# Kernel optimization log

Hardware: AMD Instinct MI355X
Metric: run time of the kernel (lower is better)

## Reference

```python
import jax, jax.numpy as jnp
import numpy as np

DILATIONS = [1, 2, 4, 8, 16, 32, 64, 128, 256, 512] * 2
WD = 128   # residual/gate channels
SD = 512   # skip channels
VOCAB = 256
FIELD = int(np.sum(DILATIONS)) + 2  # receptive field = 2048


def setup_inputs() -> dict:
    key = jax.random.key(0)
    ks = jax.random.split(key, 10)
    B, T = 4, 16384
    L = len(DILATIONS)
    y = jax.random.randint(ks[0], (B, T), 0, VOCAB)
    embed = jax.random.normal(ks[1], (VOCAB, WD), dtype=jnp.float32) * 0.1
    # dilated causal conv: kernel_size=2, wd -> 2*wd (gate stacking)
    Wd = jax.random.normal(ks[2], (L, 2 * WD, WD, 2), dtype=jnp.float32) * 0.05
    bd = jnp.zeros((L, 2 * WD), dtype=jnp.float32)
    # skip 1x1 conv: wd -> sd
    Ws = jax.random.normal(ks[3], (L, SD, WD, 1), dtype=jnp.float32) * 0.05
    bs = jnp.zeros((L, SD), dtype=jnp.float32)
    # residual 1x1 conv: wd -> wd
    Wr = jax.random.normal(ks[4], (L, WD, WD, 1), dtype=jnp.float32) * 0.05
    br = jnp.zeros((L, WD), dtype=jnp.float32)
    # post convs (bias=False)
    W1 = jax.random.normal(ks[5], (SD, SD, 1), dtype=jnp.float32) * 0.05
    W2 = jax.random.normal(ks[6], (VOCAB, SD, 1), dtype=jnp.float32) * 0.05
    return {"y": y, "embed": embed, "Wd": Wd, "bd": bd, "Ws": Ws,
            "bs": bs, "Wr": Wr, "br": br, "W1": W1, "W2": W2}


def reference(y, embed, Wd, bd, Ws, bs, Wr, br, W1, W2):
    # embedding -> [B, C, T]
    x = jnp.transpose(embed[y], (0, 2, 1))
    finalout = x.shape[2] - (FIELD - 1)
    skip = None
    for i, d in enumerate(DILATIONS):
        # dilated valid conv with kernel size 2 == two shifted 1x1 matmuls
        in_act = (jnp.einsum('oc,bct->bot', Wd[i, :, :, 0], x[:, :, :-d]) +
                  jnp.einsum('oc,bct->bot', Wd[i, :, :, 1], x[:, :, d:]) +
                  bd[i][None, :, None])                       # [B, 2*WD, T-d]
        acts = jnp.tanh(in_act[:, :WD]) * jax.nn.sigmoid(in_act[:, WD:])
        res = jnp.einsum('oc,bct->bot', Wr[i, :, :, 0], acts) + br[i][None, :, None]
        sk = (jnp.einsum('oc,bct->bot', Ws[i, :, :, 0], acts[:, :, -finalout:]) +
              bs[i][None, :, None])                            # [B, SD, finalout]
        skip = sk if skip is None else skip + sk
        x = res + x[:, :, d:]
    out = jax.nn.relu(skip)
    out = jax.nn.relu(jnp.einsum('oc,bct->bot', W1[:, :, 0], out))
    out = jnp.einsum('oc,bct->bot', W2[:, :, 0], out)          # [B, 256, finalout]
    return out
```

## Files before the change

### kernel.cpp

```cpp
#include <hip/hip_runtime.h>
#include <cstddef>

#define B_    4
#define T_    16384
#define FOUT_ 14337
#define FOUTP 14464
#define NL_   20
#define XSTR  ((size_t)T_*128)
#define ABSTR ((size_t)FOUTP*128)
#define ALSTR ((size_t)B_*FOUTP*128)
#define SBSTR ((size_t)FOUTP*512)

typedef float    f32x16 __attribute__((ext_vector_type(16)));
typedef _Float16 f16x8  __attribute__((ext_vector_type(8)));

__device__ _Float16 g_xh0[(size_t)B_*T_*128];
__device__ _Float16 g_xh1[(size_t)B_*T_*128];
__device__ _Float16 g_WdF0[(size_t)NL_*256*128];
__device__ _Float16 g_WdF1[(size_t)NL_*256*128];
__device__ _Float16 g_WrF [(size_t)NL_*128*128];
__device__ _Float16 g_WsF [(size_t)512*2560];
__device__ _Float16 g_W1F [(size_t)512*512];
__device__ _Float16 g_W2F [(size_t)256*512];
__device__ float    g_bssum[512];
__device__ _Float16 g_acts[(size_t)NL_*B_*FOUTP*128];
__device__ _Float16 g_skipF[(size_t)B_*FOUTP*512];
__device__ _Float16 g_h1F [(size_t)B_*FOUTP*512];

__device__ __forceinline__ float sigm_(float x){ return 1.0f/(1.0f+__expf(-x)); }
__device__ __forceinline__ float tanh_(float x){ return 1.0f - 2.0f/(__expf(2.0f*x)+1.0f); }
__device__ __forceinline__ f32x16 MFMA32(f16x8 a, f16x8 b, f32x16 c){
  return __builtin_amdgcn_mfma_f32_32x32x16_f16(a, b, c, 0, 0, 0);
}

typedef const __attribute__((address_space(1))) _Float16 gash;
typedef __attribute__((address_space(3))) _Float16 lash;
__device__ __forceinline__ void gld_lds16(const _Float16* g, _Float16* l){
  __builtin_amdgcn_global_load_lds((gash*)g, (lash*)l, 16, 0, 0);
}

__global__ void cvt_wd(const float* __restrict__ Wd){
  int i = blockIdx.x*256 + threadIdx.x;
  if (i >= NL_*256*16) return;
  int row = i >> 4, koct = i & 15;
  const float* s = Wd + ((size_t)row*128 + koct*8)*2;
  int lane = (koct&1)*32 + (row&31);
  size_t addr = (size_t)((row>>5)*8 + (koct>>1))*512 + lane*8;
  union { _Float16 h[8]; uint4 v; } u0, u1;
#pragma unroll
  for (int j=0;j<8;j++){ u0.h[j]=(_Float16)s[2*j]; u1.h[j]=(_Float16)s[2*j+1]; }
  *(uint4*)((void*)(g_WdF0 + addr)) = u0.v;
  *(uint4*)((void*)(g_WdF1 + addr)) = u1.v;
}
__global__ void cvt_rm(const float* __restrict__ src, int which, int M, int K){
  int i = blockIdx.x*256 + threadIdx.x;
  if (i >= M*(K>>3)) return;
  int row = i / (K>>3), koct = i % (K>>3);
  const float* s = src + (size_t)row*K + koct*8;
  int lane = (koct&1)*32 + (row&31);
  size_t addr = ((size_t)(row>>5)*(K>>4) + (koct>>1))*512 + lane*8;
  union { _Float16 h[8]; uint4 v; } u;
#pragma unroll
  for (int j=0;j<8;j++) u.h[j]=(_Float16)s[j];
  _Float16* dst = (which==0)?g_WrF:(which==1)?g_W1F:g_W2F;
  *(uint4*)((void*)(dst + addr)) = u.v;
}
__global__ void cvt_ws(const float* __restrict__ Ws){
  int i = blockIdx.x*256 + threadIdx.x;
  if (i >= NL_*512*16) return;
  int l = i >> 13, o = (i>>4)&511, coct = i&15;
  const float* s = Ws + ((size_t)(l*512+o))*128 + coct*8;
  int lane = (coct&1)*32 + (o&31);
  size_t addr = ((size_t)(o>>5)*160 + (size_t)(l*8 + (coct>>1)))*512 + lane*8;
  union { _Float16 h[8]; uint4 v; } u;
#pragma unroll
  for (int j=0;j<8;j++) u.h[j]=(_Float16)s[j];
  *(uint4*)((void*)(g_WsF + addr)) = u.v;
}
__global__ void bssum_k(const float* __restrict__ bs){
  int o = threadIdx.x;
  float s = 0.f;
  for (int l=0;l<NL_;l++) s += bs[l*512 + o];
  g_bssum[o] = s;
}

__global__ void embed_kernel(const int* __restrict__ y, const float* __restrict__ embed){
  int gid = blockIdx.x*256 + threadIdx.x;
  int bt = gid >> 4, c8 = gid & 15;
  if (bt < B_*T_){
    int idx = y[bt];
    const float* e = embed + (size_t)idx*128 + c8*8;
    union { _Float16 h[8]; uint4 v; } u;
#pragma unroll
    for (int j=0;j<8;j++) u.h[j]=(_Float16)e[j];
    *(uint4*)((void*)(g_xh0 + (size_t)bt*128 + c8*8)) = u.v;
  }
}

__global__ __launch_bounds__(256,2) void layer16(
    int swap, int l, int d, int Tout, int ss,
    const float* __restrict__ bd_l, const float* __restrict__ br_l)
{
  const _Float16* __restrict__ xin  = swap ? g_xh1 : g_xh0;
  _Float16* __restrict__       xout = swap ? g_xh0 : g_xh1;

  __shared__ _Float16 X0s[16*520];
  __shared__ _Float16 X1s[16*520];
  __shared__ _Float16 ACs[16*520];

  const int tid = threadIdx.x;
  const int w   = tid >> 6;
  const int lane= tid & 63;
  const int ln2 = lane & 31;
  const int h   = lane >> 5;
  const int b   = blockIdx.y;
  const int t0  = blockIdx.x*64;
  const int ntv = min(64, Tout - t0);
  const int limit = Tout + d - 1;
  const _Float16* __restrict__ xb = xin + (size_t)b*XSTR;

#pragma unroll
  for (int it=0; it<4; it++){
    int t = (tid>>4) + it*16, c16 = tid&15;
    int s0 = t0 + t;     if (s0 > limit) s0 = limit;
    int s1 = t0 + t + d; if (s1 > limit) s1 = limit;
    *(uint4*)((void*)&X0s[c16*520 + t*8]) = *(const uint4*)((const void*)(xb + (size_t)s0*128 + c16*8));
    *(uint4*)((void*)&X1s[c16*520 + t*8]) = *(const uint4*)((const void*)(xb + (size_t)s1*128 + c16*8));
  }
  __syncthreads();

  f32x16 aB[2][2];
#pragma unroll
  for (int mi=0;mi<2;mi++)
#pragma unroll
    for (int nt=0;nt<2;nt++)
#pragma unroll
      for (int r=0;r<16;r++) aB[mi][nt][r] = 0.f;

#pragma unroll
  for (int tap=0; tap<2; tap++){
    const _Float16* __restrict__ Xs = tap ? X1s : X0s;
    const _Float16* __restrict__ Wt = (tap ? g_WdF1 : g_WdF0) + (size_t)l*32768;
    const _Float16* aT = Wt + (size_t)w*4096 + lane*8;
    const _Float16* aS = Wt + (size_t)(4+w)*4096 + lane*8;
#pragma unroll
    for (int ks=0; ks<8; ks++){
      f16x8 bfr[2];
#pragma unroll
      for (int nt=0; nt<2; nt++)
        bfr[nt] = *(const f16x8*)((const void*)&Xs[(ks*2+h)*520 + (nt*32+ln2)*8]);
      f16x8 fT = *(const f16x8*)((const void*)(aT + ks*512));
      f16x8 fS = *(const f16x8*)((const void*)(aS + ks*512));
#pragma unroll
      for (int nt=0; nt<2; nt++){
        aB[0][nt] = MFMA32(fT, bfr[nt], aB[0][nt]);
        aB[1][nt] = MFMA32(fS, bfr[nt], aB[1][nt]);
      }
    }
  }

#pragma unroll
  for (int nt=0; nt<2; nt++)
#pragma unroll
    for (int rq=0; rq<4; rq++){
      int c0 = w*32 + rq*8 + 4*h;
      union { _Float16 hh[4]; ushort4 v; } pk;
#pragma unroll
      for (int rr=0; rr<4; rr++){
        float it_ = aB[0][nt][rq*4+rr] + bd_l[c0+rr];
        float is_ = aB[1][nt][rq*4+rr] + bd_l[128+c0+rr];
        pk.hh[rr] = (_Float16)(tanh_(it_)*sigm_(is_));
      }
      *(ushort4*)((void*)&ACs[(w*4+rq)*520 + (nt*32+ln2)*8 + 4*h]) = pk.v;
    }
  __syncthreads();

  f32x16 aC[2];
#pragma unroll
  for (int nt=0;nt<2;nt++)
#pragma unroll
    for (int r=0;r<16;r++) aC[nt][r] = 0.f;
  {
    const _Float16* aW = g_WrF + (size_t)l*16384 + (size_t)w*4096 + lane*8;
#pragma unroll
    for (int ks=0; ks<8; ks++){
      f16x8 bfr[2];
#pragma unroll
      for (int nt=0; nt<2; nt++)
        bfr[nt] = *(const f16x8*)((const void*)&ACs[(ks*2+h)*520 + (nt*32+ln2)*8]);
      f16x8 fW = *(const f16x8*)((const void*)(aW + ks*512));
#pragma unroll
      for (int nt=0; nt<2; nt++)
        aC[nt] = MFMA32(fW, bfr[nt], aC[nt]);
    }
  }

#pragma unroll
  for (int nt=0; nt<2; nt++){
    int t = nt*32 + ln2;
    if (t < ntv){
      size_t xrow = (size_t)b*XSTR + (size_t)(t0+t)*128;
#pragma unroll
      for (int rq=0; rq<4; rq++){
        int c0 = w*32 + rq*8 + 4*h;
        union { ushort4 v; _Float16 hh[4]; } xr;
        xr.v = *(const ushort4*)((const void*)&X1s[(w*4+rq)*520 + t*8 + 4*h]);
        union { _Float16 hh[4]; ushort4 v; } ov;
#pragma unroll
        for (int rr=0; rr<4; rr++)
          ov.hh[rr] = (_Float16)(aC[nt][rq*4+rr] + br_l[c0+rr] + (float)xr.hh[rr]);
        *(ushort4*)((void*)(xout + xrow + c0)) = ov.v;
      }
    }
  }

  _Float16* __restrict__ actsB = g_acts + (size_t)l*ALSTR + (size_t)b*ABSTR;
#pragma unroll
  for (int it=0; it<4; it++){
    int t = (tid>>4) + it*16, c16 = tid&15;
    int ts = t0 + t - ss;
    if (t < ntv && ts >= 0 && ts < FOUT_){
      size_t addr = (size_t)(ts>>5)*4096 + (size_t)(c16>>1)*512 + ((c16&1)*32 + (ts&31))*8;
      *(uint4*)((void*)(actsB + addr)) = *(const uint4*)((const void*)&ACs[c16*520 + t*8]);
    }
  }
}

template<int MODE>
__global__ __launch_bounds__(512,4) void gemm_stream(float* __restrict__ outF){
  constexpr int NSTEP = (MODE==0)?160:32;
  constexpr int NSC   = NSTEP/4;
  const _Float16* __restrict__ A    = (MODE==0)?g_WsF:(MODE==1)?g_W1F:g_W2F;
  const _Float16* __restrict__ Bsrc = (MODE==0)?g_acts:(MODE==1)?g_skipF:g_h1F;

  __shared__ __align__(16) _Float16 Bs[4][8192];

  const int tid = threadIdx.x;
  const int w   = tid >> 6;
  const int lane= tid & 63;
  const int ln2 = lane & 31;
  const int h   = lane >> 5;

  int lin = blockIdx.x;
  int mhalf, pairIdx;
  if (MODE==2){ mhalf = 0; pairIdx = lin; }
  else {
    mhalf   = (lin>>3)&1;
    pairIdx = ((lin>>4)<<3) | (lin&7);
    if (pairIdx >= 452) return;
  }
  const int b    = pairIdx / 113;
  const int tsb  = pairIdx - b*113;
  const int ts0  = tsb*128;
  const int mtile= mhalf*8 + w;

  const _Float16* Gq[2];
#pragma unroll
  for (int q=0;q<2;q++){
    int nt = (w*2+q)&3;
    size_t tile = (size_t)tsb*4 + nt;
    Gq[q] = (MODE==0) ? (Bsrc + (size_t)b*ABSTR + tile*4096  + lane*8)
                      : (Bsrc + (size_t)b*SBSTR + tile*16384 + lane*8);
  }

  const _Float16* Aw = A + (size_t)mtile*((size_t)NSTEP*512) + lane*8;

  f32x16 acc[4];
#pragma unroll
  for (int nt=0;nt<4;nt++)
#pragma unroll
    for (int r=0;r<16;r++) acc[nt][r] = 0.f;

  auto STAGE = [&](int buf, int sc){
#pragma unroll
    for (int q=0;q<2;q++){
      int bi   = w*2 + q;
      int kslq = bi>>2;
      const _Float16* g;
      if (MODE==0){
        int ks = sc*4 + kslq;
        g = Gq[q] + (size_t)(ks>>3)*ALSTR + (size_t)(ks&7)*512;
      } else {
        g = Gq[q] + (size_t)(sc*4 + kslq)*512;
      }
      gld_lds16(g, &Bs[buf][(size_t)bi*512]);
    }
  };

  STAGE(0,0);
  STAGE(1,1);
  asm volatile("s_waitcnt vmcnt(2)" ::: "memory");
  __builtin_amdgcn_sched_barrier(0);
  __builtin_amdgcn_s_barrier();

  for (int c=0; c<NSC; ++c){
    const int buf = c & 3;
    f16x8 af[4];
#pragma unroll
    for (int j=0;j<4;j++)
      af[j] = *(const f16x8*)((const void*)(Aw + (size_t)(c*4+j)*512));
    __builtin_amdgcn_sched_barrier(0);
    if (c+2 < NSC) STAGE((c+2)&3, c+2);
    __builtin_amdgcn_sched_barrier(0);
    __builtin_amdgcn_s_setprio(1);
#pragma unroll
    for (int j=0;j<4;j++){
      f16x8 bfr[4];
#pragma unroll
      for (int nt=0;nt<4;nt++)
        bfr[nt] = *(const f16x8*)((const void*)&Bs[buf][(size_t)(j*4+nt)*512 + lane*8]);
#pragma unroll
      for (int nt=0;nt<4;nt++)
        acc[nt] = MFMA32(af[j], bfr[nt], acc[nt]);
    }
    __builtin_amdgcn_s_setprio(0);
    __builtin_amdgcn_sched_barrier(0);
    __builtin_amdgcn_s_barrier();
  }

  if (MODE != 2){
    _Float16* __restrict__ dstb = ((MODE==0)?g_skipF:g_h1F) + (size_t)b*SBSTR;
#pragma unroll
    for (int nt=0; nt<4; nt++){
      int ts = ts0 + nt*32 + ln2;
      if (ts >= FOUT_) continue;
#pragma unroll
      for (int rq=0; rq<4; rq++){
        int m0 = mtile*32 + rq*8 + 4*h;
        union { _Float16 hh[4]; ushort4 v; } pk;
#pragma unroll
        for (int rr=0; rr<4; rr++){
          float vv = acc[nt][rq*4+rr];
          if (MODE==0) vv += g_bssum[m0+rr];
          pk.hh[rr] = (_Float16)fmaxf(vv, 0.f);
        }
        size_t addr = (size_t)(ts>>5)*16384 + (size_t)(mtile*2 + (rq>>1))*512
                    + ((rq&1)*32 + (ts&31))*8 + 4*h;
        *(ushort4*)((void*)(dstb + addr)) = pk.v;
      }
    }
  } else {
#pragma unroll
    for (int nt=0; nt<4; nt++){
      int ts = ts0 + nt*32 + ln2;
      if (ts >= FOUT_) continue;
#pragma unroll
      for (int rq=0; rq<4; rq++){
        int m0 = w*32 + rq*8 + 4*h;
#pragma unroll
        for (int rr=0; rr<4; rr++)
          outF[((size_t)(b*256 + m0 + rr))*FOUT_ + ts] = acc[nt][rq*4+rr];
      }
    }
  }
}

extern "C" void kernel_launch(void* const* d_in, const int* in_sizes, int n_in,
                              void* d_out, int out_size, void* d_ws, size_t ws_size,
                              hipStream_t stream) {
  const int*   y     = (const int*)  d_in[0];
  const float* embed = (const float*)d_in[1];
  const float* Wd    = (const float*)d_in[2];
  const float* bd    = (const float*)d_in[3];
  const float* Ws    = (const float*)d_in[4];
  const float* bs    = (const float*)d_in[5];
  const float* Wr    = (const float*)d_in[6];
  const float* br    = (const float*)d_in[7];
  const float* W1    = (const float*)d_in[8];
  const float* W2    = (const float*)d_in[9];
  float* out = (float*)d_out;
  (void)d_ws; (void)ws_size;

  cvt_wd<<<dim3(320), dim3(256), 0, stream>>>(Wd);
  cvt_rm<<<dim3(160), dim3(256), 0, stream>>>(Wr, 0, NL_*128, 128);
  cvt_rm<<<dim3(128), dim3(256), 0, stream>>>(W1, 1, 512, 512);
  cvt_rm<<<dim3( 64), dim3(256), 0, stream>>>(W2, 2, 256, 512);
  cvt_ws<<<dim3(640), dim3(256), 0, stream>>>(Ws);
  bssum_k<<<dim3(1), dim3(512), 0, stream>>>(bs);

  embed_kernel<<<dim3((B_*T_*16)/256), dim3(256), 0, stream>>>(y, embed);

  static const int DIL[NL_] = {1,2,4,8,16,32,64,128,256,512,
                               1,2,4,8,16,32,64,128,256,512};
  int swap = 0;
  int Tin = T_;
  for (int i=0;i<NL_;i++){
    int d = DIL[i];
    int Tout = Tin - d;
    dim3 grid((Tout+63)/64, B_);
    layer16<<<grid, dim3(256), 0, stream>>>(
        swap, i, d, Tout, Tout - FOUT_, bd + (size_t)i*256, br + (size_t)i*128);
    swap ^= 1;
    Tin = Tout;
  }

  gemm_stream<0><<<dim3(928), dim3(512), 0, stream>>>(nullptr);
  gemm_stream<1><<<dim3(928), dim3(512), 0, stream>>>(nullptr);
  gemm_stream<2><<<dim3(452), dim3(512), 0, stream>>>(out);
}
```

Before: 950.9 us.

## Fuse twenty layer launches into one persistent kernel with grid barriers

Replaces the per-layer kernel launches with a single persistent kernel of 512 blocks that loops over all 20 layers, striding over tiles and synchronising between layers with a software grid barrier built on atomics. This removes launch overhead and tail gaps between the layer kernels. In exchange, a spin barrier adds latency at every layer boundary. The barrier also depends on all 512 blocks being resident at once, with occupancy raised to 3 blocks per CU, and has a timeout guard that could silently break correctness.

Result: slower. 3.313 ms (+248.4%).

```diff
diff --git a/kernel.cpp b/kernel.cpp
--- a/kernel.cpp
+++ b/kernel.cpp
@@ -10,6 +10,7 @@
 #define ABSTR ((size_t)FOUTP*128)
 #define ALSTR ((size_t)B_*FOUTP*128)
 #define SBSTR ((size_t)FOUTP*512)
+#define NBLK_ 512
 
 typedef float    f32x16 __attribute__((ext_vector_type(16)));
 typedef _Float16 f16x8  __attribute__((ext_vector_type(8)));
@@ -27,6 +28,12 @@
 __device__ _Float16 g_skipF[(size_t)B_*FOUTP*512];
 __device__ _Float16 g_h1F [(size_t)B_*FOUTP*512];
 
+__device__ unsigned g_bcnt = 0;
+__device__ unsigned g_bgen = 0;
+
+__constant__ int c_DIL[NL_] = {1,2,4,8,16,32,64,128,256,512,
+                               1,2,4,8,16,32,64,128,256,512};
+
 __device__ __forceinline__ float sigm_(float x){ return 1.0f/(1.0f+__expf(-x)); }
 __device__ __forceinline__ float tanh_(float x){ return 1.0f - 2.0f/(__expf(2.0f*x)+1.0f); }
 __device__ __forceinline__ f32x16 MFMA32(f16x8 a, f16x8 b, f32x16 c){
@@ -37,6 +44,21 @@
 typedef __attribute__((address_space(3))) _Float16 lash;
 __device__ __forceinline__ void gld_lds16(const _Float16* g, _Float16* l){
   __builtin_amdgcn_global_load_lds((gash*)g, (lash*)l, 16, 0, 0);
+}
+
+__device__ __forceinline__ void grid_barrier(){
+  unsigned gen = __hip_atomic_load(&g_bgen, __ATOMIC_ACQUIRE, __HIP_MEMORY_SCOPE_AGENT);
+  unsigned old = __hip_atomic_fetch_add(&g_bcnt, 1u, __ATOMIC_ACQ_REL, __HIP_MEMORY_SCOPE_AGENT);
+  if (old == (unsigned)(NBLK_ - 1)){
+    __hip_atomic_store(&g_bcnt, 0u, __ATOMIC_RELAXED, __HIP_MEMORY_SCOPE_AGENT);
+    __hip_atomic_fetch_add(&g_bgen, 1u, __ATOMIC_RELEASE, __HIP_MEMORY_SCOPE_AGENT);
+  } else {
+    unsigned guard = 0;
+    while (__hip_atomic_load(&g_bgen, __ATOMIC_ACQUIRE, __HIP_MEMORY_SCOPE_AGENT) == gen){
+      __builtin_amdgcn_s_sleep(8);
+      if (++guard > 40000000u) break;
+    }
+  }
 }
 
 __global__ void cvt_wd(const float* __restrict__ Wd){
@@ -97,13 +119,9 @@
   }
 }
 
-__global__ __launch_bounds__(256,2) void layer16(
-    int swap, int l, int d, int Tout, int ss,
-    const float* __restrict__ bd_l, const float* __restrict__ br_l)
+__global__ __launch_bounds__(256,3) void layer_chain(
+    const float* __restrict__ bd, const float* __restrict__ br)
 {
-  const _Float16* __restrict__ xin  = swap ? g_xh1 : g_xh0;
-  _Float16* __restrict__       xout = swap ? g_xh0 : g_xh1;
-
   __shared__ _Float16 X0s[16*520];
   __shared__ _Float16 X1s[16*520];
   __shared__ _Float16 ACs[16*520];
@@ -113,116 +131,142 @@
   const int lane= tid & 63;
   const int ln2 = lane & 31;
   const int h   = lane >> 5;
-  const int b   = blockIdx.y;
-  const int t0  = blockIdx.x*64;
-  const int ntv = min(64, Tout - t0);
-  const int limit = Tout + d - 1;
-  const _Float16* __restrict__ xb = xin + (size_t)b*XSTR;
-
-#pragma unroll
-  for (int it=0; it<4; it++){
-    int t = (tid>>4) + it*16, c16 = tid&15;
-    int s0 = t0 + t;     if (s0 > limit) s0 = limit;
-    int s1 = t0 + t + d; if (s1 > limit) s1 = limit;
-    *(uint4*)((void*)&X0s[c16*520 + t*8]) = *(const uint4*)((const void*)(xb + (size_t)s0*128 + c16*8));
-    *(uint4*)((void*)&X1s[c16*520 + t*8]) = *(const uint4*)((const void*)(xb + (size_t)s1*128 + c16*8));
-  }
-  __syncthreads();
-
-  f32x16 aB[2][2];
-#pragma unroll
-  for (int mi=0;mi<2;mi++)
-#pragma unroll
-    for (int nt=0;nt<2;nt++)
-#pragma unroll
-      for (int r=0;r<16;r++) aB[mi][nt][r] = 0.f;
-
-#pragma unroll
-  for (int tap=0; tap<2; tap++){
-    const _Float16* __restrict__ Xs = tap ? X1s : X0s;
-    const _Float16* __restrict__ Wt = (tap ? g_WdF1 : g_WdF0) + (size_t)l*32768;
-    const _Float16* aT = Wt + (size_t)w*4096 + lane*8;
-    const _Float16* aS = Wt + (size_t)(4+w)*4096 + lane*8;
-#pragma unroll
-    for (int ks=0; ks<8; ks++){
-      f16x8 bfr[2];
+
+  int Tin  = T_;
+  int swap = 0;
+
+  for (int l = 0; l < NL_; ++l){
+    const int d     = c_DIL[l];
+    const int Tout  = Tin - d;
+    const int ss    = Tout - FOUT_;
+    const int limit = Tout + d - 1;
+    const _Float16* __restrict__ xin  = swap ? g_xh1 : g_xh0;
+    _Float16* __restrict__       xout = swap ? g_xh0 : g_xh1;
+    const float* __restrict__ bd_l = bd + (size_t)l*256;
+    const float* __restrict__ br_l = br + (size_t)l*128;
+    const int nxt   = (Tout + 63) >> 6;
+    const int ntile = nxt * B_;
+
+    for (int tile = blockIdx.x; tile < ntile; tile += NBLK_){
+      const int b  = tile / nxt;
+      const int t0 = (tile - b*nxt) * 64;
+      const int ntv = min(64, Tout - t0);
+      const _Float16* __restrict__ xb = xin + (size_t)b*XSTR;
+
+#pragma unroll
+      for (int it=0; it<4; it++){
+        int t = (tid>>4) + it*16, c16 = tid&15;
+        int s0 = t0 + t;     if (s0 > limit) s0 = limit;
+        int s1 = t0 + t + d; if (s1 > limit) s1 = limit;
+        *(uint4*)((void*)&X0s[c16*520 + t*8]) = *(const uint4*)((const void*)(xb + (size_t)s0*128 + c16*8));
+        *(uint4*)((void*)&X1s[c16*520 + t*8]) = *(const uint4*)((const void*)(xb + (size_t)s1*128 + c16*8));
+      }
+      __syncthreads();
+
+      f32x16 aB[2][2];
+#pragma unroll
+      for (int mi=0;mi<2;mi++)
+#pragma unroll
+        for (int nt=0;nt<2;nt++)
+#pragma unroll
+          for (int r=0;r<16;r++) aB[mi][nt][r] = 0.f;
+
+#pragma unroll
+      for (int tap=0; tap<2; tap++){
+        const _Float16* __restrict__ Xs = tap ? X1s : X0s;
+        const _Float16* __restrict__ Wt = (tap ? g_WdF1 : g_WdF0) + (size_t)l*32768;
+        const _Float16* aT = Wt + (size_t)w*4096 + lane*8;
+        const _Float16* aS = Wt + (size_t)(4+w)*4096 + lane*8;
+#pragma unroll
+        for (int ks=0; ks<8; ks++){
+          f16x8 bfr[2];
+#pragma unroll
+          for (int nt=0; nt<2; nt++)
+            bfr[nt] = *(const f16x8*)((const void*)&Xs[(ks*2+h)*520 + (nt*32+ln2)*8]);
+          f16x8 fT = *(const f16x8*)((const void*)(aT + ks*512));
+          f16x8 fS = *(const f16x8*)((const void*)(aS + ks*512));
+#pragma unroll
+          for (int nt=0; nt<2; nt++){
+            aB[0][nt] = MFMA32(fT, bfr[nt], aB[0][nt]);
+            aB[1][nt] = MFMA32(fS, bfr[nt], aB[1][nt]);
+          }
+        }
+      }
+
 #pragma unroll
       for (int nt=0; nt<2; nt++)
-        bfr[nt] = *(const f16x8*)((const void*)&Xs[(ks*2+h)*520 + (nt*32+ln2)*8]);
-      f16x8 fT = *(const f16x8*)((const void*)(aT + ks*512));
-      f16x8 fS = *(const f16x8*)((const void*)(aS + ks*512));
+#pragma unroll
+        for (int rq=0; rq<4; rq++){
+          int c0 = w*32 + rq*8 + 4*h;
+          union { _Float16 hh[4]; ushort4 v; } pk;
+#pragma unroll
+          for (int rr=0; rr<4; rr++){
+            float it_ = aB[0][nt][rq*4+rr] + bd_l[c0+rr];
+            float is_ = aB[1][nt][rq*4+rr] + bd_l[128+c0+rr];
+            pk.hh[rr] = (_Float16)(tanh_(it_)*sigm_(is_));
+          }
+          *(ushort4*)((void*)&ACs[(w*4+rq)*520 + (nt*32+ln2)*8 + 4*h]) = pk.v;
+        }
+      __syncthreads();
+
+      f32x16 aC[2];
+#pragma unroll
+      for (int nt=0;nt<2;nt++)
+#pragma unroll
+        for (int r=0;r<16;r++) aC[nt][r] = 0.f;
+      {
+        const _Float16* aW = g_WrF + (size_t)l*16384 + (size_t)w*4096 + lane*8;
+#pragma unroll
+        for (int ks=0; ks<8; ks++){
+          f16x8 bfr[2];
+#pragma unroll
+          for (int nt=0; nt<2; nt++)
+            bfr[nt] = *(const f16x8*)((const void*)&ACs[(ks*2+h)*520 + (nt*32+ln2)*8]);
+          f16x8 fW = *(const f16x8*)((const void*)(aW + ks*512));
+#pragma unroll
+          for (int nt=0; nt<2; nt++)
+            aC[nt] = MFMA32(fW, bfr[nt], aC[nt]);
+        }
+      }
+
 #pragma unroll
       for (int nt=0; nt<2; nt++){
-        aB[0][nt] = MFMA32(fT, bfr[nt], aB[0][nt]);
-        aB[1][nt] = MFMA32(fS, bfr[nt], aB[1][nt]);
-      }
-    }
-  }
-
-#pragma unroll
-  for (int nt=0; nt<2; nt++)
-#pragma unroll
-    for (int rq=0; rq<4; rq++){
-      int c0 = w*32 + rq*8 + 4*h;
-      union { _Float16 hh[4]; ushort4 v; } pk;
-#pragma unroll
-      for (int rr=0; rr<4; rr++){
-        float it_ = aB[0][nt][rq*4+rr] + bd_l[c0+rr];
-        float is_ = aB[1][nt][rq*4+rr] + bd_l[128+c0+rr];
-        pk.hh[rr] = (_Float16)(tanh_(it_)*sigm_(is_));
-      }
-      *(ushort4*)((void*)&ACs[(w*4+rq)*520 + (nt*32+ln2)*8 + 4*h]) = pk.v;
-    }
-  __syncthreads();
-
-  f32x16 aC[2];
-#pragma unroll
-  for (int nt=0;nt<2;nt++)
-#pragma unroll
-    for (int r=0;r<16;r++) aC[nt][r] = 0.f;
-  {
-    const _Float16* aW = g_WrF + (size_t)l*16384 + (size_t)w*4096 + lane*8;
-#pragma unroll
-    for (int ks=0; ks<8; ks++){
-      f16x8 bfr[2];
-#pragma unroll
-      for (int nt=0; nt<2; nt++)
-        bfr[nt] = *(const f16x8*)((const void*)&ACs[(ks*2+h)*520 + (nt*32+ln2)*8]);
-      f16x8 fW = *(const f16x8*)((const void*)(aW + ks*512));
-#pragma unroll
-      for (int nt=0; nt<2; nt++)
-        aC[nt] = MFMA32(fW, bfr[nt], aC[nt]);
-    }
-  }
-
-#pragma unroll
-  for (int nt=0; nt<2; nt++){
-    int t = nt*32 + ln2;
-    if (t < ntv){
-      size_t xrow = (size_t)b*XSTR + (size_t)(t0+t)*128;
-#pragma unroll
-      for (int rq=0; rq<4; rq++){
-        int c0 = w*32 + rq*8 + 4*h;
-        union { ushort4 v; _Float16 hh[4]; } xr;
-        xr.v = *(const ushort4*)((const void*)&X1s[(w*4+rq)*520 + t*8 + 4*h]);
-        union { _Float16 hh[4]; ushort4 v; } ov;
-#pragma unroll
-        for (int rr=0; rr<4; rr++)
-          ov.hh[rr] = (_Float16)(aC[nt][rq*4+rr] + br_l[c0+rr] + (float)xr.hh[rr]);
-        *(ushort4*)((void*)(xout + xrow + c0)) = ov.v;
-      }
-    }
-  }
-
-  _Float16* __restrict__ actsB = g_acts + (size_t)l*ALSTR + (size_t)b*ABSTR;
-#pragma unroll
-  for (int it=0; it<4; it++){
-    int t = (tid>>4) + it*16, c16 = tid&15;
-    int ts = t0 + t - ss;
-    if (t < ntv && ts >= 0 && ts < FOUT_){
-      size_t addr = (size_t)(ts>>5)*4096 + (size_t)(c16>>1)*512 + ((c16&1)*32 + (ts&31))*8;
-      *(uint4*)((void*)(actsB + addr)) = *(const uint4*)((const void*)&ACs[c16*520 + t*8]);
-    }
+        int t = nt*32 + ln2;
+        if (t < ntv){
+          size_t xrow = (size_t)b*XSTR + (size_t)(t0+t)*128;
+#pragma unroll
+          for (int rq=0; rq<4; rq++){
+            int c0 = w*32 + rq*8 + 4*h;
+            union { ushort4 v; _Float16 hh[4]; } xr;
+            xr.v = *(const ushort4*)((const void*)&X1s[(w*4+rq)*520 + t*8 + 4*h]);
+            union { _Float16 hh[4]; ushort4 v; } ov;
+#pragma unroll
+            for (int rr=0; rr<4; rr++)
+              ov.hh[rr] = (_Float16)(aC[nt][rq*4+rr] + br_l[c0+rr] + (float)xr.hh[rr]);
+            *(ushort4*)((void*)(xout + xrow + c0)) = ov.v;
+          }
+        }
+      }
+
+      _Float16* __restrict__ actsB = g_acts + (size_t)l*ALSTR + (size_t)b*ABSTR;
+#pragma unroll
+      for (int it=0; it<4; it++){
+        int t = (tid>>4) + it*16, c16 = tid&15;
+        int ts = t0 + t - ss;
+        if (t < ntv && ts >= 0 && ts < FOUT_){
+          size_t addr = (size_t)(ts>>5)*4096 + (size_t)(c16>>1)*512 + ((c16&1)*32 + (ts&31))*8;
+          *(uint4*)((void*)(actsB + addr)) = *(const uint4*)((const void*)&ACs[c16*520 + t*8]);
+        }
+      }
+      __syncthreads();
+    }
+
+    __syncthreads();
+    if (tid == 0) grid_barrier();
+    __syncthreads();
+
+    swap ^= 1;
+    Tin = Tout;
   }
 }
 
@@ -380,19 +424,7 @@
 
   embed_kernel<<<dim3((B_*T_*16)/256), dim3(256), 0, stream>>>(y, embed);
 
-  static const int DIL[NL_] = {1,2,4,8,16,32,64,128,256,512,
-                               1,2,4,8,16,32,64,128,256,512};
-  int swap = 0;
-  int Tin = T_;
-  for (int i=0;i<NL_;i++){
-    int d = DIL[i];
-    int Tout = Tin - d;
-    dim3 grid((Tout+63)/64, B_);
-    layer16<<<grid, dim3(256), 0, stream>>>(
-        swap, i, d, Tout, Tout - FOUT_, bd + (size_t)i*256, br + (size_t)i*128);
-    swap ^= 1;
-    Tin = Tout;
-  }
+  layer_chain<<<dim3(NBLK_), dim3(256), 0, stream>>>(bd, br);
 
   gemm_stream<0><<<dim3(928), dim3(512), 0, stream>>>(nullptr);
   gemm_stream<1><<<dim3(928), dim3(512), 0, stream>>>(nullptr);
```
